# Kernel tuning notes

Hardware: AMD Instinct MI355X
Metric: run time of the kernel (lower is better)

## Reference

```python
import jax, jax.numpy as jnp
import numpy as np

N = 100000
E = 1600000
IN_DIM, HID_DIM, LAT_DIM = 256, 128, 64


def glorot(key, shape):
    lim = float(np.sqrt(6.0 / (shape[0] + shape[1])))
    return jax.random.uniform(key, shape, jnp.float32, -lim, lim)


def setup_inputs() -> dict:
    key = jax.random.key(0)
    ks = jax.random.split(key, 8)
    x = jax.random.normal(ks[0], (N, IN_DIM), jnp.float32)
    edge_index = jax.random.randint(ks[1], (2, E), 0, N, jnp.int64)
    return {
        "x": x,
        "edge_index": edge_index,
        "W1": glorot(ks[2], (IN_DIM, HID_DIM)),
        "b1": jnp.zeros((HID_DIM,), jnp.float32),
        "Wmu": glorot(ks[3], (HID_DIM, LAT_DIM)),
        "bmu": jnp.zeros((LAT_DIM,), jnp.float32),
        "Wls": glorot(ks[4], (HID_DIM, LAT_DIM)),
        "bls": jnp.zeros((LAT_DIM,), jnp.float32),
    }


def gcn_conv(x, src, dst, norm, W, b, n_nodes):
    # PyG GCNConv: linear transform, then symmetric-normalized scatter-add
    h = x @ W                                   # [N, out]
    msg = h[src] * norm[:, None]                # [E+N, out] gathered messages
    out = jax.ops.segment_sum(msg, dst, num_segments=n_nodes)
    return out + b


def reference(x, edge_index, W1, b1, Wmu, bmu, Wls, bls):
    # add self-loops (GCNConv default)
    loop = jnp.arange(N, dtype=edge_index.dtype)
    src = jnp.concatenate([edge_index[0], loop])
    dst = jnp.concatenate([edge_index[1], loop])
    # symmetric degree normalization: deg computed on target nodes
    deg = jax.ops.segment_sum(jnp.ones_like(dst, jnp.float32), dst, num_segments=N)
    dinv = jnp.where(deg > 0, jax.lax.rsqrt(jnp.maximum(deg, 1.0)), 0.0)
    norm = dinv[src] * dinv[dst]                # [E+N]

    h = jax.nn.relu(gcn_conv(x, src, dst, norm, W1, b1, N))
    mu = gcn_conv(h, src, dst, norm, Wmu, bmu, N)
    logstd = gcn_conv(h, src, dst, norm, Wls, bls, N)
    return (mu, logstd)
```

## Files before the change

kernel.cpp:

```cpp
#include <hip/hip_runtime.h>

#define IN_DIM 256
#define HID    128
#define LAT    64
#define SLOTS  64
#define RANGE  200
#define MAXBKT 512

typedef __attribute__((ext_vector_type(8))) short short8;
typedef __attribute__((ext_vector_type(4))) float floatx4;
typedef __attribute__((ext_vector_type(4))) int  intx4;
typedef __attribute__((ext_vector_type(2))) int  intx2;

static __device__ __forceinline__ ushort f2bf(float f) {
    union { float f; uint u; } v; v.f = f;
    uint u = v.u;
    uint r = (u + 0x7fffu + ((u >> 16) & 1u)) >> 16;
    return (ushort)r;
}
static __device__ __forceinline__ float bf_lo(uint v) { return __uint_as_float(v << 16); }
static __device__ __forceinline__ float bf_hi(uint v) { return __uint_as_float(v & 0xffff0000u); }

__global__ __launch_bounds__(256) void scatter_kernel(const int* __restrict__ src,
                                                      const int* __restrict__ dst,
                                                      int* __restrict__ bkt,
                                                      int* __restrict__ bkt_cnt,
                                                      int cap, int nbkt, int E) {
    __shared__ int cntL[MAXBKT], baseL[MAXBKT], posL[MAXBKT];
    const int t = threadIdx.x;
    for (int b = t; b < nbkt; b += 256) { cntL[b] = 0; posL[b] = 0; }
    __syncthreads();
    const int e0 = blockIdx.x * 2048 + t * 8;
    int s[8], d[8];
    if (e0 + 7 < E) {
        *(int4*)(s)     = *(const int4*)(src + e0);
        *(int4*)(s + 4) = *(const int4*)(src + e0 + 4);
        *(int4*)(d)     = *(const int4*)(dst + e0);
        *(int4*)(d + 4) = *(const int4*)(dst + e0 + 4);
    } else {
        #pragma unroll
        for (int k = 0; k < 8; ++k) {
            int e = e0 + k;
            s[k] = (e < E) ? src[e] : 0;
            d[k] = (e < E) ? dst[e] : -1;
        }
    }
    int r[8];
    #pragma unroll
    for (int k = 0; k < 8; ++k) {
        r[k] = (d[k] >= 0) ? (d[k] / RANGE) : -1;
        if (r[k] >= 0) atomicAdd(&cntL[r[k]], 1);
    }
    __syncthreads();
    for (int b = t; b < nbkt; b += 256) {
        int c = cntL[b];
        baseL[b] = c ? atomicAdd(&bkt_cnt[b], c) : 0;
    }
    __syncthreads();
    #pragma unroll
    for (int k = 0; k < 8; ++k) {
        if (r[k] >= 0) {
            int off = atomicAdd(&posL[r[k]], 1);
            int p = baseL[r[k]] + off;
            if (p < cap) {
                intx2 pk; pk.x = s[k]; pk.y = d[k];
                __builtin_nontemporal_store(pk,
                    (intx2*)(bkt + ((size_t)r[k] * cap + p) * 2));
            }
        }
    }
}

__global__ __launch_bounds__(256) void fill_bin_kernel(const int* __restrict__ bkt,
                                                       const int* __restrict__ bkt_cnt,
                                                       int* __restrict__ cur,
                                                       int* __restrict__ csr,
                                                       int cap, int N) {
    __shared__ int lcnt[RANGE];
    __shared__ int lslots[RANGE * SLOTS];
    const int r  = blockIdx.x;
    const int lo = r * RANGE;
    const int R  = min(RANGE, N - lo);
    if (R <= 0) return;
    for (int j = threadIdx.x; j < R; j += 256) lcnt[j] = 0;
    __syncthreads();
    const int sz = min(bkt_cnt[r], cap);
    const int* b = bkt + (size_t)r * cap * 2;
    for (int i = threadIdx.x; i < sz; i += 256) {
        intx2 e = __builtin_nontemporal_load((const intx2*)(b + (size_t)i * 2));
        int ln = e.y - lo;
        int p = atomicAdd(&lcnt[ln], 1);
        if (p < SLOTS) lslots[(ln << 6) + p] = e.x;
    }
    __syncthreads();
    const int nInt4 = R << 4;
    int4* dstp = (int4*)(csr + ((size_t)lo << 6));
    const int4* srcp = (const int4*)lslots;
    for (int j = threadIdx.x; j < nInt4; j += 256)
        dstp[j] = srcp[j];
    for (int j = threadIdx.x; j < R; j += 256)
        cur[lo + j] = lcnt[j];
}

__global__ __launch_bounds__(256) void dinv_kernel(const int* __restrict__ cur,
                                                   float* __restrict__ dinv, int N) {
    int i = blockIdx.x * 256 + threadIdx.x;
    if (i < N) dinv[i] = rsqrtf((float)(cur[i] + 1));
}

__global__ void prep_weights(const float* __restrict__ W1, const float* __restrict__ Wmu,
                             const float* __restrict__ Wls,
                             ushort* __restrict__ W1T, ushort* __restrict__ W2T) {
    int idx = blockIdx.x * 256 + threadIdx.x;
    if (idx < IN_DIM * HID) {
        int n = idx & 127, k = idx >> 7;
        W1T[n * IN_DIM + k] = f2bf(W1[idx]);
    } else {
        int j = idx - IN_DIM * HID;
        if (j < HID * LAT) {
            int n = j & 63, k = j >> 6;
            W2T[n * HID + k] = f2bf(Wmu[j]);
        } else {
            int jj = j - HID * LAT;
            int n = jj & 63, k = jj >> 6;
            W2T[(64 + n) * HID + k] = f2bf(Wls[jj]);
        }
    }
}

__global__ __launch_bounds__(256) void gemm1_mfma(const float* __restrict__ X,
                                                  const ushort* __restrict__ W1T,
                                                  ushort* __restrict__ O, int N) {
    __shared__ ushort As[64 * 32];
    __shared__ ushort Bs[128 * 32];
    __shared__ ushort Cs[64 * 128];
    const int tid  = threadIdx.x;
    const int wave = tid >> 6, lane = tid & 63;
    const int q = lane >> 4, ln = lane & 15;
    const int row0 = blockIdx.x * 64;
    floatx4 acc[8] = {};

    for (int k0 = 0; k0 < IN_DIM; k0 += 32) {
        #pragma unroll
        for (int t = 0; t < 2; ++t) {
            int j = t * 256 + tid;
            int r = j >> 3, kc = (j & 7) * 4;
            float4 v = make_float4(0.f, 0.f, 0.f, 0.f);
            if (row0 + r < N)
                v = *(const float4*)(X + (size_t)(row0 + r) * IN_DIM + k0 + kc);
            *(ushort4*)(As + r * 32 + kc) =
                make_ushort4(f2bf(v.x), f2bf(v.y), f2bf(v.z), f2bf(v.w));
        }
        #pragma unroll
        for (int t = 0; t < 2; ++t) {
            int c = t * 256 + tid;
            int n = c >> 2, kc = (c & 3) * 8;
            *(int4*)(Bs + n * 32 + kc) = *(const int4*)(W1T + (size_t)n * IN_DIM + k0 + kc);
        }
        __syncthreads();
        short8 a = *(const short8*)(As + (wave * 16 + ln) * 32 + q * 8);
        #pragma unroll
        for (int t = 0; t < 8; ++t) {
            short8 b = *(const short8*)(Bs + (t * 16 + ln) * 32 + q * 8);
            acc[t] = __builtin_amdgcn_mfma_f32_16x16x32_bf16(a, b, acc[t], 0, 0, 0);
        }
        __syncthreads();
    }
    #pragma unroll
    for (int t = 0; t < 8; ++t)
        #pragma unroll
        for (int r = 0; r < 4; ++r)
            Cs[(wave * 16 + q * 4 + r) * 128 + t * 16 + ln] = f2bf(acc[t][r]);
    __syncthreads();
    #pragma unroll
    for (int t = 0; t < 4; ++t) {
        int j = t * 256 + tid;
        int r = j >> 4, c8 = (j & 15) * 8;
        if (row0 + r < N)
            *(int4*)(O + (size_t)(row0 + r) * HID + c8) = *(const int4*)(Cs + r * 128 + c8);
    }
}

__global__ __launch_bounds__(256) void agg_kernel(const ushort* __restrict__ in,
                                                  ushort* __restrict__ out,
                                                  const int* __restrict__ cnt,
                                                  const int* __restrict__ csr,
                                                  const float* __restrict__ dinv,
                                                  const float* __restrict__ bias,
                                                  int N, int mode) {
    int wid  = (blockIdx.x * 256 + threadIdx.x) >> 6;
    int lane = threadIdx.x & 63;
    if (wid >= N) return;
    const int cn   = min(cnt[wid], SLOTS);
    const float dd = dinv[wid];
    int e    = (cn > 0) ? csr[(wid << 6) + min(lane, cn - 1)] : wid;
    float nr = dinv[e] * dd;
    const int q    = lane >> 4;
    const int boff = (lane & 15) * 8;
    const ushort* inb = in + boff;
    float a0=0.f,a1=0.f,a2=0.f,a3=0.f,a4=0.f,a5=0.f,a6=0.f,a7=0.f;
    const int nfull = cn >> 2;
    int jj = 0;
    for (; jj + 2 <= nfull; jj += 2) {
        int j0 = (jj << 2) + q, j1 = j0 + 4;
        int   s0 = __shfl(e,  j0);
        int   s1 = __shfl(e,  j1);
        float n0 = __shfl(nr, j0);
        float n1 = __shfl(nr, j1);
        uint4 v0 = *(const uint4*)(inb + (size_t)s0 * HID);
        uint4 v1 = *(const uint4*)(inb + (size_t)s1 * HID);
        a0 += bf_lo(v0.x) * n0; a1 += bf_hi(v0.x) * n0;
        a2 += bf_lo(v0.y) * n0; a3 += bf_hi(v0.y) * n0;
        a4 += bf_lo(v0.z) * n0; a5 += bf_hi(v0.z) * n0;
        a6 += bf_lo(v0.w) * n0; a7 += bf_hi(v0.w) * n0;
        a0 += bf_lo(v1.x) * n1; a1 += bf_hi(v1.x) * n1;
        a2 += bf_lo(v1.y) * n1; a3 += bf_hi(v1.y) * n1;
        a4 += bf_lo(v1.z) * n1; a5 += bf_hi(v1.z) * n1;
        a6 += bf_lo(v1.w) * n1; a7 += bf_hi(v1.w) * n1;
    }
    if (jj < nfull) {
        int j0 = (jj << 2) + q;
        int   s0 = __shfl(e,  j0);
        float n0 = __shfl(nr, j0);
        uint4 v0 = *(const uint4*)(inb + (size_t)s0 * HID);
        a0 += bf_lo(v0.x) * n0; a1 += bf_hi(v0.x) * n0;
        a2 += bf_lo(v0.y) * n0; a3 += bf_hi(v0.y) * n0;
        a4 += bf_lo(v0.z) * n0; a5 += bf_hi(v0.z) * n0;
        a6 += bf_lo(v0.w) * n0; a7 += bf_hi(v0.w) * n0;
    }
    {
        int rem = cn - (nfull << 2);
        int jT  = max(min((nfull << 2) + q, cn - 1), 0);
        int   sT = __shfl(e,  jT);
        float nT = __shfl(nr, jT);
        if (q < rem) {
            uint4 v0 = *(const uint4*)(inb + (size_t)sT * HID);
            a0 += bf_lo(v0.x) * nT; a1 += bf_hi(v0.x) * nT;
            a2 += bf_lo(v0.y) * nT; a3 += bf_hi(v0.y) * nT;
            a4 += bf_lo(v0.z) * nT; a5 += bf_hi(v0.z) * nT;
            a6 += bf_lo(v0.w) * nT; a7 += bf_hi(v0.w) * nT;
        }
    }
    a0 += __shfl_xor(a0, 16); a1 += __shfl_xor(a1, 16);
    a2 += __shfl_xor(a2, 16); a3 += __shfl_xor(a3, 16);
    a4 += __shfl_xor(a4, 16); a5 += __shfl_xor(a5, 16);
    a6 += __shfl_xor(a6, 16); a7 += __shfl_xor(a7, 16);
    a0 += __shfl_xor(a0, 32); a1 += __shfl_xor(a1, 32);
    a2 += __shfl_xor(a2, 32); a3 += __shfl_xor(a3, 32);
    a4 += __shfl_xor(a4, 32); a5 += __shfl_xor(a5, 32);
    a6 += __shfl_xor(a6, 32); a7 += __shfl_xor(a7, 32);
    if (q == 0) {
        {
            uint4 sv = *(const uint4*)(in + (size_t)wid * HID + boff);
            float ss = dd * dd;
            a0 += bf_lo(sv.x) * ss; a1 += bf_hi(sv.x) * ss;
            a2 += bf_lo(sv.y) * ss; a3 += bf_hi(sv.y) * ss;
            a4 += bf_lo(sv.z) * ss; a5 += bf_hi(sv.z) * ss;
            a6 += bf_lo(sv.w) * ss; a7 += bf_hi(sv.w) * ss;
        }
        if (mode) {
            float4 b0 = *(const float4*)(bias + boff);
            float4 b1 = *(const float4*)(bias + boff + 4);
            a0 = fmaxf(a0 + b0.x, 0.f); a1 = fmaxf(a1 + b0.y, 0.f);
            a2 = fmaxf(a2 + b0.z, 0.f); a3 = fmaxf(a3 + b0.w, 0.f);
            a4 = fmaxf(a4 + b1.x, 0.f); a5 = fmaxf(a5 + b1.y, 0.f);
            a6 = fmaxf(a6 + b1.z, 0.f); a7 = fmaxf(a7 + b1.w, 0.f);
        }
        uint4 pk;
        pk.x = (uint)f2bf(a0) | ((uint)f2bf(a1) << 16);
        pk.y = (uint)f2bf(a2) | ((uint)f2bf(a3) << 16);
        pk.z = (uint)f2bf(a4) | ((uint)f2bf(a5) << 16);
        pk.w = (uint)f2bf(a6) | ((uint)f2bf(a7) << 16);
        *(uint4*)(out + (size_t)wid * HID + boff) = pk;
    }
}

__global__ __launch_bounds__(256) void gemm2_mfma(const ushort* __restrict__ G,
                                                  const ushort* __restrict__ W2T,
                                                  const float* __restrict__ bmu,
                                                  const float* __restrict__ bls,
                                                  float* __restrict__ mu,
                                                  float* __restrict__ ls, int N) {
    __shared__ ushort As[64 * 32];
    __shared__ ushort Bs[128 * 32];
    __shared__ float  Cs[64 * 128];
    const int tid  = threadIdx.x;
    const int wave = tid >> 6, lane = tid & 63;
    const int q = lane >> 4, ln = lane & 15;
    const int row0 = blockIdx.x * 64;
    floatx4 acc[8] = {};

    for (int k0 = 0; k0 < HID; k0 += 32) {
        {
            int r = tid >> 2, kc = (tid & 3) * 8;
            int4 v = make_int4(0, 0, 0, 0);
            if (row0 + r < N) v = *(const int4*)(G + (size_t)(row0 + r) * HID + k0 + kc);
            *(int4*)(As + r * 32 + kc) = v;
        }
        #pragma unroll
        for (int t = 0; t < 2; ++t) {
            int c = t * 256 + tid;
            int n = c >> 2, kc = (c & 3) * 8;
            *(int4*)(Bs + n * 32 + kc) = *(const int4*)(W2T + (size_t)n * HID + k0 + kc);
        }
        __syncthreads();
        short8 a = *(const short8*)(As + (wave * 16 + ln) * 32 + q * 8);
        #pragma unroll
        for (int t = 0; t < 8; ++t) {
            short8 b = *(const short8*)(Bs + (t * 16 + ln) * 32 + q * 8);
            acc[t] = __builtin_amdgcn_mfma_f32_16x16x32_bf16(a, b, acc[t], 0, 0, 0);
        }
        __syncthreads();
    }
    #pragma unroll
    for (int t = 0; t < 8; ++t)
        #pragma unroll
        for (int r = 0; r < 4; ++r)
            Cs[(wave * 16 + q * 4 + r) * 128 + t * 16 + ln] = acc[t][r];
    __syncthreads();
    #pragma unroll
    for (int t = 0; t < 8; ++t) {
        int j = t * 256 + tid;
        int r = j >> 5, c4 = (j & 31) * 4;
        if (row0 + r < N) {
            float4 v = *(const float4*)(Cs + r * 128 + c4);
            if (c4 < 64) {
                float4 b = *(const float4*)(bmu + c4);
                *(float4*)(mu + (size_t)(row0 + r) * LAT + c4) =
                    make_float4(v.x + b.x, v.y + b.y, v.z + b.z, v.w + b.w);
            } else {
                float4 b = *(const float4*)(bls + (c4 - 64));
                *(float4*)(ls + (size_t)(row0 + r) * LAT + (c4 - 64)) =
                    make_float4(v.x + b.x, v.y + b.y, v.z + b.z, v.w + b.w);
            }
        }
    }
}

extern "C" void kernel_launch(void* const* d_in, const int* in_sizes, int n_in,
                              void* d_out, int out_size, void* d_ws, size_t ws_size,
                              hipStream_t stream) {
    const float* x    = (const float*)d_in[0];
    const int*   edge = (const int*)d_in[1];
    const float* W1   = (const float*)d_in[2];
    const float* b1   = (const float*)d_in[3];
    const float* Wmu  = (const float*)d_in[4];
    const float* bmu  = (const float*)d_in[5];
    const float* Wls  = (const float*)d_in[6];
    const float* bls  = (const float*)d_in[7];

    const int N    = in_sizes[0] / IN_DIM;
    const int E    = in_sizes[1] / 2;
    const int nbkt = (N + RANGE - 1) / RANGE;
    const int cap  = 4096;

    const int* src = edge;
    const int* dst = edge + E;

    ushort* t1b  = (ushort*)d_ws;
    ushort* hb   = t1b + (size_t)N * HID;
    int*    csr  = (int*)(hb + (size_t)N * HID);
    int*    bkt  = (int*)(csr + (size_t)N * SLOTS);
    float*  dinv = (float*)(bkt + (size_t)MAXBKT * cap * 2);
    int*    cur  = (int*)(dinv + N);
    int* bkt_cnt = cur + N;
    ushort* W1T  = (ushort*)(bkt_cnt + MAXBKT);
    ushort* W2T  = W1T + IN_DIM * HID;
    ushort* gb   = t1b;

    float* mu = (float*)d_out;
    float* ls = mu + (size_t)N * LAT;

    (void)hipMemsetAsync(bkt_cnt, 0, (size_t)MAXBKT * sizeof(int), stream);

    scatter_kernel<<<(E + 2047) / 2048, 256, 0, stream>>>(src, dst, bkt, bkt_cnt, cap, nbkt, E);
    fill_bin_kernel<<<nbkt, 256, 0, stream>>>(bkt, bkt_cnt, cur, csr, cap, N);
    dinv_kernel<<<(N + 255) / 256, 256, 0, stream>>>(cur, dinv, N);

    prep_weights<<<(IN_DIM * HID + 2 * HID * LAT) / 256, 256, 0, stream>>>(W1, Wmu, Wls, W1T, W2T);
    gemm1_mfma<<<(N + 63) / 64, 256, 0, stream>>>(x, W1T, t1b, N);

    {
        int blocks = (int)(((long long)N * 64 + 255) / 256);
        agg_kernel<<<blocks, 256, 0, stream>>>(t1b, hb, cur, csr, dinv, b1, N, 1);
    }
    {
        int blocks = (int)(((long long)N * 64 + 255) / 256);
        agg_kernel<<<blocks, 256, 0, stream>>>(hb, gb, cur, csr, dinv, nullptr, N, 0);
    }

    gemm2_mfma<<<(N + 63) / 64, 256, 0, stream>>>(gb, W2T, bmu, bls, mu, ls, N);
}
```

Baseline: 412.1 us.

## Merge edge scatter with first GEMM in one launch and fold dinv into binning

The edge bucketing scatter and the first feature GEMM now run in a single launch, with the block index picking which job each block does, so the two independent stages can overlap on the GPU. The separate dinv kernel is removed and its rsqrt is computed in the fill_bin epilogue. Bucket stores switch from nontemporal to normal stores. The shared 28KB union buffer may reduce occupancy for scatter blocks, and the mixed workload may load-balance unevenly.

```diff
diff --git a/kernel.cpp b/kernel.cpp
--- a/kernel.cpp
+++ b/kernel.cpp
@@ -21,59 +21,117 @@
 static __device__ __forceinline__ float bf_lo(uint v) { return __uint_as_float(v << 16); }
 static __device__ __forceinline__ float bf_hi(uint v) { return __uint_as_float(v & 0xffff0000u); }
 
-__global__ __launch_bounds__(256) void scatter_kernel(const int* __restrict__ src,
-                                                      const int* __restrict__ dst,
-                                                      int* __restrict__ bkt,
-                                                      int* __restrict__ bkt_cnt,
-                                                      int cap, int nbkt, int E) {
-    __shared__ int cntL[MAXBKT], baseL[MAXBKT], posL[MAXBKT];
-    const int t = threadIdx.x;
-    for (int b = t; b < nbkt; b += 256) { cntL[b] = 0; posL[b] = 0; }
-    __syncthreads();
-    const int e0 = blockIdx.x * 2048 + t * 8;
-    int s[8], d[8];
-    if (e0 + 7 < E) {
-        *(int4*)(s)     = *(const int4*)(src + e0);
-        *(int4*)(s + 4) = *(const int4*)(src + e0 + 4);
-        *(int4*)(d)     = *(const int4*)(dst + e0);
-        *(int4*)(d + 4) = *(const int4*)(dst + e0 + 4);
-    } else {
+__global__ __launch_bounds__(256) void scatter_gemm1_kernel(
+        const int* __restrict__ src, const int* __restrict__ dst,
+        int* __restrict__ bkt, int* __restrict__ bkt_cnt,
+        int cap, int nbkt, int E, int sblocks,
+        const float* __restrict__ X, const ushort* __restrict__ W1T,
+        ushort* __restrict__ O, int N) {
+    __shared__ __align__(16) char smem[28 * 1024];
+
+    if ((int)blockIdx.x < sblocks) {
+        int* cntL  = (int*)smem;
+        int* baseL = cntL + MAXBKT;
+        int* posL  = baseL + MAXBKT;
+        const int t = threadIdx.x;
+        for (int b = t; b < nbkt; b += 256) { cntL[b] = 0; posL[b] = 0; }
+        __syncthreads();
+        const int e0 = blockIdx.x * 2048 + t * 8;
+        int s[8], d[8];
+        if (e0 + 7 < E) {
+            *(int4*)(s)     = *(const int4*)(src + e0);
+            *(int4*)(s + 4) = *(const int4*)(src + e0 + 4);
+            *(int4*)(d)     = *(const int4*)(dst + e0);
+            *(int4*)(d + 4) = *(const int4*)(dst + e0 + 4);
+        } else {
+            #pragma unroll
+            for (int k = 0; k < 8; ++k) {
+                int e = e0 + k;
+                s[k] = (e < E) ? src[e] : 0;
+                d[k] = (e < E) ? dst[e] : -1;
+            }
+        }
+        int r[8];
         #pragma unroll
         for (int k = 0; k < 8; ++k) {
-            int e = e0 + k;
-            s[k] = (e < E) ? src[e] : 0;
-            d[k] = (e < E) ? dst[e] : -1;
-        }
-    }
-    int r[8];
+            r[k] = (d[k] >= 0) ? (d[k] / RANGE) : -1;
+            if (r[k] >= 0) atomicAdd(&cntL[r[k]], 1);
+        }
+        __syncthreads();
+        for (int b = t; b < nbkt; b += 256) {
+            int c = cntL[b];
+            baseL[b] = c ? atomicAdd(&bkt_cnt[b], c) : 0;
+        }
+        __syncthreads();
+        #pragma unroll
+        for (int k = 0; k < 8; ++k) {
+            if (r[k] >= 0) {
+                int off = atomicAdd(&posL[r[k]], 1);
+                int p = baseL[r[k]] + off;
+                if (p < cap) {
+                    *(intx2*)(bkt + ((size_t)r[k] * cap + p) * 2) =
+                        (intx2){s[k], d[k]};
+                }
+            }
+        }
+        return;
+    }
+
+    ushort* As = (ushort*)smem;
+    ushort* Bs = As + 64 * 32;
+    ushort* Cs = Bs + 128 * 32;
+    const int bid  = blockIdx.x - sblocks;
+    const int tid  = threadIdx.x;
+    const int wave = tid >> 6, lane = tid & 63;
+    const int q = lane >> 4, ln = lane & 15;
+    const int row0 = bid * 64;
+    floatx4 acc[8] = {};
+
+    for (int k0 = 0; k0 < IN_DIM; k0 += 32) {
+        #pragma unroll
+        for (int t = 0; t < 2; ++t) {
+            int j = t * 256 + tid;
+            int r = j >> 3, kc = (j & 7) * 4;
+            float4 v = make_float4(0.f, 0.f, 0.f, 0.f);
+            if (row0 + r < N)
+                v = *(const float4*)(X + (size_t)(row0 + r) * IN_DIM + k0 + kc);
+            *(ushort4*)(As + r * 32 + kc) =
+                make_ushort4(f2bf(v.x), f2bf(v.y), f2bf(v.z), f2bf(v.w));
+        }
+        #pragma unroll
+        for (int t = 0; t < 2; ++t) {
+            int c = t * 256 + tid;
+            int n = c >> 2, kc = (c & 3) * 8;
+            *(int4*)(Bs + n * 32 + kc) = *(const int4*)(W1T + (size_t)n * IN_DIM + k0 + kc);
+        }
+        __syncthreads();
+        short8 a = *(const short8*)(As + (wave * 16 + ln) * 32 + q * 8);
+        #pragma unroll
+        for (int t = 0; t < 8; ++t) {
+            short8 b = *(const short8*)(Bs + (t * 16 + ln) * 32 + q * 8);
+            acc[t] = __builtin_amdgcn_mfma_f32_16x16x32_bf16(a, b, acc[t], 0, 0, 0);
+        }
+        __syncthreads();
+    }
     #pragma unroll
-    for (int k = 0; k < 8; ++k) {
-        r[k] = (d[k] >= 0) ? (d[k] / RANGE) : -1;
-        if (r[k] >= 0) atomicAdd(&cntL[r[k]], 1);
-    }
-    __syncthreads();
-    for (int b = t; b < nbkt; b += 256) {
-        int c = cntL[b];
-        baseL[b] = c ? atomicAdd(&bkt_cnt[b], c) : 0;
-    }
+    for (int t = 0; t < 8; ++t)
+        #pragma unroll
+        for (int r = 0; r < 4; ++r)
+            Cs[(wave * 16 + q * 4 + r) * 128 + t * 16 + ln] = f2bf(acc[t][r]);
     __syncthreads();
     #pragma unroll
-    for (int k = 0; k < 8; ++k) {
-        if (r[k] >= 0) {
-            int off = atomicAdd(&posL[r[k]], 1);
-            int p = baseL[r[k]] + off;
-            if (p < cap) {
-                intx2 pk; pk.x = s[k]; pk.y = d[k];
-                __builtin_nontemporal_store(pk,
-                    (intx2*)(bkt + ((size_t)r[k] * cap + p) * 2));
-            }
-        }
+    for (int t = 0; t < 4; ++t) {
+        int j = t * 256 + tid;
+        int r = j >> 4, c8 = (j & 15) * 8;
+        if (row0 + r < N)
+            *(int4*)(O + (size_t)(row0 + r) * HID + c8) = *(const int4*)(Cs + r * 128 + c8);
     }
 }
 
 __global__ __launch_bounds__(256) void fill_bin_kernel(const int* __restrict__ bkt,
                                                        const int* __restrict__ bkt_cnt,
                                                        int* __restrict__ cur,
+                                                       float* __restrict__ dinv,
                                                        int* __restrict__ csr,
                                                        int cap, int N) {
     __shared__ int lcnt[RANGE];
@@ -98,14 +156,11 @@
     const int4* srcp = (const int4*)lslots;
     for (int j = threadIdx.x; j < nInt4; j += 256)
         dstp[j] = srcp[j];
-    for (int j = threadIdx.x; j < R; j += 256)
-        cur[lo + j] = lcnt[j];
-}
-
-__global__ __launch_bounds__(256) void dinv_kernel(const int* __restrict__ cur,
-                                                   float* __restrict__ dinv, int N) {
-    int i = blockIdx.x * 256 + threadIdx.x;
-    if (i < N) dinv[i] = rsqrtf((float)(cur[i] + 1));
+    for (int j = threadIdx.x; j < R; j += 256) {
+        int c = lcnt[j];
+        cur[lo + j]  = c;
+        dinv[lo + j] = rsqrtf((float)(c + 1));
+    }
 }
 
 __global__ void prep_weights(const float* __restrict__ W1, const float* __restrict__ Wmu,
@@ -125,59 +180,6 @@
             int n = jj & 63, k = jj >> 6;
             W2T[(64 + n) * HID + k] = f2bf(Wls[jj]);
         }
-    }
-}
-
-__global__ __launch_bounds__(256) void gemm1_mfma(const float* __restrict__ X,
-                                                  const ushort* __restrict__ W1T,
-                                                  ushort* __restrict__ O, int N) {
-    __shared__ ushort As[64 * 32];
-    __shared__ ushort Bs[128 * 32];
-    __shared__ ushort Cs[64 * 128];
-    const int tid  = threadIdx.x;
-    const int wave = tid >> 6, lane = tid & 63;
-    const int q = lane >> 4, ln = lane & 15;
-    const int row0 = blockIdx.x * 64;
-    floatx4 acc[8] = {};
-
-    for (int k0 = 0; k0 < IN_DIM; k0 += 32) {
-        #pragma unroll
-        for (int t = 0; t < 2; ++t) {
-            int j = t * 256 + tid;
-            int r = j >> 3, kc = (j & 7) * 4;
-            float4 v = make_float4(0.f, 0.f, 0.f, 0.f);
-            if (row0 + r < N)
-                v = *(const float4*)(X + (size_t)(row0 + r) * IN_DIM + k0 + kc);
-            *(ushort4*)(As + r * 32 + kc) =
-                make_ushort4(f2bf(v.x), f2bf(v.y), f2bf(v.z), f2bf(v.w));
-        }
-        #pragma unroll
-        for (int t = 0; t < 2; ++t) {
-            int c = t * 256 + tid;
-            int n = c >> 2, kc = (c & 3) * 8;
-            *(int4*)(Bs + n * 32 + kc) = *(const int4*)(W1T + (size_t)n * IN_DIM + k0 + kc);
-        }
-        __syncthreads();
-        short8 a = *(const short8*)(As + (wave * 16 + ln) * 32 + q * 8);
-        #pragma unroll
-        for (int t = 0; t < 8; ++t) {
-            short8 b = *(const short8*)(Bs + (t * 16 + ln) * 32 + q * 8);
-            acc[t] = __builtin_amdgcn_mfma_f32_16x16x32_bf16(a, b, acc[t], 0, 0, 0);
-        }
-        __syncthreads();
-    }
-    #pragma unroll
-    for (int t = 0; t < 8; ++t)
-        #pragma unroll
-        for (int r = 0; r < 4; ++r)
-            Cs[(wave * 16 + q * 4 + r) * 128 + t * 16 + ln] = f2bf(acc[t][r]);
-    __syncthreads();
-    #pragma unroll
-    for (int t = 0; t < 4; ++t) {
-        int j = t * 256 + tid;
-        int r = j >> 4, c8 = (j & 15) * 8;
-        if (row0 + r < N)
-            *(int4*)(O + (size_t)(row0 + r) * HID + c8) = *(const int4*)(Cs + r * 128 + c8);
     }
 }
 
@@ -373,12 +375,16 @@
 
     (void)hipMemsetAsync(bkt_cnt, 0, (size_t)MAXBKT * sizeof(int), stream);
 
-    scatter_kernel<<<(E + 2047) / 2048, 256, 0, stream>>>(src, dst, bkt, bkt_cnt, cap, nbkt, E);
-    fill_bin_kernel<<<nbkt, 256, 0, stream>>>(bkt, bkt_cnt, cur, csr, cap, N);
-    dinv_kernel<<<(N + 255) / 256, 256, 0, stream>>>(cur, dinv, N);
-
     prep_weights<<<(IN_DIM * HID + 2 * HID * LAT) / 256, 256, 0, stream>>>(W1, Wmu, Wls, W1T, W2T);
-    gemm1_mfma<<<(N + 63) / 64, 256, 0, stream>>>(x, W1T, t1b, N);
+
+    {
+        int sblocks  = (E + 2047) / 2048;
+        int g1blocks = (N + 63) / 64;
+        scatter_gemm1_kernel<<<sblocks + g1blocks, 256, 0, stream>>>(
+            src, dst, bkt, bkt_cnt, cap, nbkt, E, sblocks, x, W1T, t1b, N);
+    }
+
+    fill_bin_kernel<<<nbkt, 256, 0, stream>>>(bkt, bkt_cnt, cur, dinv, csr, cap, N);
 
     {
         int blocks = (int)(((long long)N * 64 + 255) / 256);
```

After: 374.0 us. 1.1x faster.
